# Performance work log

Measured on AMD Instinct MI355X. Metric: run time of the kernel, lower is better.

## Reference

```python
import jax, jax.numpy as jnp
import numpy as np

N = 50000   # nodes
E = 600000  # edges
D = 128     # embedding_dim
L = 4       # num_message_passing_steps


def setup_inputs() -> dict:
    key = jax.random.key(0)
    ks = jax.random.split(key, 5)
    x = jax.random.normal(ks[0], (N, D), dtype=jnp.float32)
    edge_index = jax.random.randint(ks[1], (2, E), 0, N, dtype=jnp.int32)
    # Per-layer params: MPNN linear (no bias), GCNConv weight + bias.
    lin_w = jax.random.normal(ks[2], (L, D, D), dtype=jnp.float32) / np.sqrt(D).astype(np.float32)
    gcn_w = jax.random.normal(ks[3], (L, D, D), dtype=jnp.float32) / np.sqrt(D).astype(np.float32)
    gcn_b = jax.random.normal(ks[4], (L, D), dtype=jnp.float32) * 0.01
    return {"x": x, "edge_index": edge_index, "lin_w": lin_w, "gcn_w": gcn_w, "gcn_b": gcn_b}


def reference(x, edge_index, lin_w, gcn_w, gcn_b):
    n = x.shape[0]
    # GCNConv defaults: add_self_loops=True, normalize=True.
    loops = jnp.arange(n, dtype=edge_index.dtype)
    src = jnp.concatenate([edge_index[0], loops])  # [E+N]
    dst = jnp.concatenate([edge_index[1], loops])  # [E+N]
    # Degree computed on dst (col) for flow='source_to_target'.
    deg = jax.ops.segment_sum(jnp.ones_like(src, dtype=x.dtype), dst, num_segments=n)
    dinv = jnp.where(deg > 0, jax.lax.rsqrt(jnp.maximum(deg, 1.0)), 0.0)
    norm = dinv[src] * dinv[dst]  # [E+N]

    for l in range(lin_w.shape[0]):
        h = x @ lin_w[l].T                 # MPNNLayer.linear (no bias)
        h = h @ gcn_w[l].T                 # GCNConv internal linear
        msgs = h[src] * norm[:, None]      # gather + normalize  [E+N, D]
        agg = jax.ops.segment_sum(msgs, dst, num_segments=n)
        x = agg + gcn_b[l]                 # GCNConv bias
        # NOTE: self.relu is `Sequential as ReLU` -> empty Sequential = identity.
    return x
```

## Files before the change

### kernel.cpp

```cpp
#include <hip/hip_runtime.h>

#define DEMB 128

typedef __attribute__((ext_vector_type(8))) _Float16 half8;
typedef __attribute__((ext_vector_type(4))) _Float16 half4;
typedef __attribute__((ext_vector_type(4))) float f32x4;

__global__ void kwc(const float* __restrict__ gcn, const float* __restrict__ lin,
                    float* __restrict__ Ms) {
  __shared__ float sa[128];
  int l = blockIdx.x >> 7, i = blockIdx.x & 127, j = threadIdx.x;
  sa[j] = gcn[((size_t)l * 128 + i) * 128 + j];
  __syncthreads();
  float acc = 0.f;
#pragma unroll 8
  for (int k = 0; k < 128; ++k) acc += sa[k] * lin[((size_t)l * 128 + k) * 128 + j];
  Ms[((size_t)l * 128 + i) * 128 + j] = acc;
}

__global__ void kst2(const float* __restrict__ Ms, const float* __restrict__ gb,
                     float* __restrict__ A1, float* __restrict__ B1,
                     float* __restrict__ v0, float* __restrict__ cb) {
  const float* M0 = Ms;
  const float* M1 = Ms + 16384;
  const float* M2 = Ms + 2 * 16384;
  const float* M3 = Ms + 3 * 16384;
  __shared__ float sa[128];
  int b = blockIdx.x, j = threadIdx.x;
  if (b < 128) {
    sa[j] = M1[b * 128 + j];
    __syncthreads();
    float acc = 0.f;
#pragma unroll 8
    for (int k = 0; k < 128; ++k) acc += sa[k] * M0[k * 128 + j];
    A1[b * 128 + j] = acc;
  } else if (b < 256) {
    int i = b - 128;
    sa[j] = M3[i * 128 + j];
    __syncthreads();
    float acc = 0.f;
#pragma unroll 8
    for (int k = 0; k < 128; ++k) acc += sa[k] * M2[k * 128 + j];
    B1[i * 128 + j] = acc;
  } else if (b == 256) {
    sa[j] = gb[j];
    __syncthreads();
    float acc = 0.f;
#pragma unroll 8
    for (int k = 0; k < 128; ++k) acc += M1[j * 128 + k] * sa[k];
    v0[j] = acc;
  } else {
    sa[j] = gb[2 * 128 + j];
    __syncthreads();
    float acc = 0.f;
#pragma unroll 8
    for (int k = 0; k < 128; ++k) acc += M3[j * 128 + k] * sa[k];
    cb[256 + j] = acc;
  }
}

__global__ void kst3(const float* __restrict__ A1, const float* __restrict__ B1,
                     const float* __restrict__ v0, const float* __restrict__ gb,
                     _Float16* __restrict__ Rh, float* __restrict__ cb) {
  __shared__ float sa[128];
  int b = blockIdx.x, j = threadIdx.x;
  if (b < 128) {
    sa[j] = B1[b * 128 + j];
    __syncthreads();
    float acc = 0.f;
#pragma unroll 8
    for (int k = 0; k < 128; ++k) acc += sa[k] * A1[k * 128 + j];
    Rh[b * 128 + j] = (_Float16)acc;
  } else if (b == 128) {
    sa[j] = v0[j];
    __syncthreads();
    float acc = 0.f;
#pragma unroll 8
    for (int k = 0; k < 128; ++k) acc += B1[j * 128 + k] * sa[k];
    cb[j] = acc;
  } else {
    sa[j] = gb[128 + j];
    __syncthreads();
    float acc = 0.f;
#pragma unroll 8
    for (int k = 0; k < 128; ++k) acc += B1[j * 128 + k] * sa[k];
    cb[128 + j] = acc;
  }
}

__global__ void kinit(int* __restrict__ deg, int n) {
  int i = blockIdx.x * 256 + threadIdx.x;
  if (i < n) deg[i] = 0;
}

__global__ void kdeg(const int* __restrict__ ei, int* __restrict__ deg, int etot) {
  int i = blockIdx.x * 256 + threadIdx.x;
  if (i < etot) atomicAdd(&deg[ei[etot + i]], 1);
}

__global__ void kscan1(const int* __restrict__ deg, int* __restrict__ off,
                       int* __restrict__ bsum, float* __restrict__ dinv,
                       float* __restrict__ dinv2, int n) {
  __shared__ int s[256];
  int t = threadIdx.x, i = blockIdx.x * 256 + t;
  int c = 0;
  if (i < n) {
    c = deg[i];
    float dv = rsqrtf((float)(c + 1));
    dinv[i] = dv;
    dinv2[i] = dv * dv;
  }
  s[t] = c;
  __syncthreads();
  for (int o = 1; o < 256; o <<= 1) {
    int v = (t >= o) ? s[t - o] : 0;
    __syncthreads();
    s[t] += v;
    __syncthreads();
  }
  if (i < n) off[i] = s[t] - c;
  if (t == 255) bsum[blockIdx.x] = s[t];
}

__global__ void kscan2(const int* __restrict__ bsum, int* __restrict__ boff,
                       int nb, int* __restrict__ off, int n, int etot) {
  __shared__ int s[256];
  int t = threadIdx.x;
  int c = (t < nb) ? bsum[t] : 0;
  s[t] = c;
  __syncthreads();
  for (int o = 1; o < 256; o <<= 1) {
    int v = (t >= o) ? s[t - o] : 0;
    __syncthreads();
    s[t] += v;
    __syncthreads();
  }
  if (t < nb) boff[t] = s[t] - c;
  if (t == 0) off[n] = etot;
}

__global__ void kscan3(int* __restrict__ off, const int* __restrict__ boff,
                       int* __restrict__ cur, int n) {
  int i = blockIdx.x * 256 + threadIdx.x;
  if (i < n) {
    int o = off[i] + boff[i >> 8];
    off[i] = o;
    cur[i] = o;
  }
}

__global__ void kfill(const int* __restrict__ ei, int* __restrict__ cur,
                      int* __restrict__ csr, int etot) {
  int i = blockIdx.x * 256 + threadIdx.x;
  if (i < etot) {
    int d = ei[etot + i];
    int p = atomicAdd(&cur[d], 1);
    csr[p] = ei[i];
  }
}

__global__ void kpre(const float* __restrict__ x, const float* __restrict__ dinv,
                     _Float16* __restrict__ xh, int n) {
  int gid = blockIdx.x * 256 + threadIdx.x;
  if (gid >= n * 32) return;
  int r = gid >> 5, c = (gid & 31) * 4;
  float d = dinv[r];
  float4 v = *(const float4*)(x + (size_t)r * DEMB + c);
  half4 o = {(_Float16)(v.x * d), (_Float16)(v.y * d), (_Float16)(v.z * d), (_Float16)(v.w * d)};
  *(half4*)(xh + (size_t)r * DEMB + c) = o;
}

template <int WITHU>
__launch_bounds__(256)
__global__ void kagg16(const _Float16* __restrict__ vin, const int* __restrict__ csr,
                       const int* __restrict__ off, const float* __restrict__ scale,
                       const float* __restrict__ dinv, const float* __restrict__ a_in,
                       float* __restrict__ u_out, float* __restrict__ a_out,
                       _Float16* __restrict__ vout, int n) {
  int node = (int)((blockIdx.x * 256u + threadIdx.x) >> 4);
  if (node >= n) return;
  int l16 = threadIdx.x & 15;
  const _Float16* base = vin + 8 * l16;
  half8 sv = *(const half8*)(base + (size_t)node * DEMB);
  float acc[8];
#pragma unroll
  for (int j = 0; j < 8; ++j) acc[j] = (float)sv[j];
  float s = WITHU ? a_in[node] : 0.f;
  int e = off[node], end = off[node + 1];
  for (; e + 8 <= end; e += 8) {
    int i0 = csr[e], i1 = csr[e + 1], i2 = csr[e + 2], i3 = csr[e + 3];
    int i4 = csr[e + 4], i5 = csr[e + 5], i6 = csr[e + 6], i7 = csr[e + 7];
    half8 r0 = *(const half8*)(base + (size_t)i0 * DEMB);
    half8 r1 = *(const half8*)(base + (size_t)i1 * DEMB);
    half8 r2 = *(const half8*)(base + (size_t)i2 * DEMB);
    half8 r3 = *(const half8*)(base + (size_t)i3 * DEMB);
    half8 r4 = *(const half8*)(base + (size_t)i4 * DEMB);
    half8 r5 = *(const half8*)(base + (size_t)i5 * DEMB);
    half8 r6 = *(const half8*)(base + (size_t)i6 * DEMB);
    half8 r7 = *(const half8*)(base + (size_t)i7 * DEMB);
    if (WITHU)
      s += a_in[i0] + a_in[i1] + a_in[i2] + a_in[i3] +
           a_in[i4] + a_in[i5] + a_in[i6] + a_in[i7];
#pragma unroll
    for (int j = 0; j < 8; ++j)
      acc[j] += ((float)r0[j] + (float)r1[j]) + ((float)r2[j] + (float)r3[j]) +
                ((float)r4[j] + (float)r5[j]) + ((float)r6[j] + (float)r7[j]);
  }
  for (; e + 4 <= end; e += 4) {
    int i0 = csr[e], i1 = csr[e + 1], i2 = csr[e + 2], i3 = csr[e + 3];
    half8 r0 = *(const half8*)(base + (size_t)i0 * DEMB);
    half8 r1 = *(const half8*)(base + (size_t)i1 * DEMB);
    half8 r2 = *(const half8*)(base + (size_t)i2 * DEMB);
    half8 r3 = *(const half8*)(base + (size_t)i3 * DEMB);
    if (WITHU) s += a_in[i0] + a_in[i1] + a_in[i2] + a_in[i3];
#pragma unroll
    for (int j = 0; j < 8; ++j)
      acc[j] += ((float)r0[j] + (float)r1[j]) + ((float)r2[j] + (float)r3[j]);
  }
  if (e < end) {
    int em = end - 1;
    int i0 = csr[e];
    int i1 = csr[min(e + 1, em)];
    int i2 = csr[min(e + 2, em)];
    float w1 = (e + 1 < end) ? 1.f : 0.f;
    float w2 = (e + 2 < end) ? 1.f : 0.f;
    half8 r0 = *(const half8*)(base + (size_t)i0 * DEMB);
    half8 r1 = *(const half8*)(base + (size_t)i1 * DEMB);
    half8 r2 = *(const half8*)(base + (size_t)i2 * DEMB);
    if (WITHU) s += a_in[i0] + w1 * a_in[i1] + w2 * a_in[i2];
#pragma unroll
    for (int j = 0; j < 8; ++j)
      acc[j] += (float)r0[j] + w1 * (float)r1[j] + w2 * (float)r2[j];
  }
  float sc = scale[node];
  half8 o;
#pragma unroll
  for (int j = 0; j < 8; ++j) o[j] = (_Float16)(acc[j] * sc);
  *(half8*)(vout + (size_t)node * DEMB + 8 * l16) = o;
  if (WITHU && l16 == 0) {
    float dv = dinv[node];
    float u = dv * s;
    u_out[node] = u;
    a_out[node] = dv * u;
  }
}

__launch_bounds__(256)
__global__ void kgemm16(const _Float16* __restrict__ y, const _Float16* __restrict__ Rh,
                        const float* __restrict__ u1, const float* __restrict__ u2,
                        const float* __restrict__ u3, const float* __restrict__ cb,
                        const float* __restrict__ b3, float* __restrict__ out, int n) {
  int t = threadIdx.x;
  int wv = t >> 6, lane = t & 63;
  int l16 = lane & 15, g = lane >> 4;
  int row0 = blockIdx.x * 128 + wv * 32;
  f32x4 acc[2][8];
#pragma unroll
  for (int w = 0; w < 2; ++w)
#pragma unroll
    for (int n8 = 0; n8 < 8; ++n8) acc[w][n8] = (f32x4){0.f, 0.f, 0.f, 0.f};

#pragma unroll
  for (int k0 = 0; k0 < 128; k0 += 32) {
    half8 a0 = *(const half8*)(y + (size_t)(row0 + l16) * DEMB + k0 + g * 8);
    half8 a1 = *(const half8*)(y + (size_t)(row0 + 16 + l16) * DEMB + k0 + g * 8);
#pragma unroll
    for (int n8 = 0; n8 < 8; ++n8) {
      half8 b = *(const half8*)(Rh + (size_t)(n8 * 16 + l16) * DEMB + k0 + g * 8);
      acc[0][n8] = __builtin_amdgcn_mfma_f32_16x16x32_f16(a0, b, acc[0][n8], 0, 0, 0);
      acc[1][n8] = __builtin_amdgcn_mfma_f32_16x16x32_f16(a1, b, acc[1][n8], 0, 0, 0);
    }
  }
#pragma unroll
  for (int n8 = 0; n8 < 8; ++n8) {
    int col = n8 * 16 + l16;
    float cA = cb[col], cB = cb[128 + col], cC = cb[256 + col], bb = b3[col];
#pragma unroll
    for (int w = 0; w < 2; ++w)
#pragma unroll
      for (int r = 0; r < 4; ++r) {
        int row = row0 + w * 16 + g * 4 + r;
        if (row < n) {
          out[(size_t)row * DEMB + col] =
              acc[w][n8][r] + u3[row] * cA + u2[row] * cB + u1[row] * cC + bb;
        }
      }
  }
}

extern "C" void kernel_launch(void* const* d_in, const int* in_sizes, int n_in,
                              void* d_out, int out_size, void* d_ws, size_t ws_size,
                              hipStream_t stream) {
  const float* x0 = (const float*)d_in[0];
  const int* ei = (const int*)d_in[1];
  const float* lin = (const float*)d_in[2];
  const float* gcn = (const float*)d_in[3];
  const float* gb = (const float*)d_in[4];
  float* out = (float*)d_out;

  int N = in_sizes[0] / DEMB;
  int E = in_sizes[1] / 2;
  int L = in_sizes[2] / (DEMB * DEMB);
  int NP = (N + 127) & ~127;

  char* w = (char*)d_ws;
  auto carve = [&](size_t bytes) {
    char* p = w;
    w += (bytes + 255) & ~(size_t)255;
    return p;
  };
  float* Ms    = (float*)carve((size_t)L * DEMB * DEMB * 4);
  float* A1    = (float*)carve((size_t)DEMB * DEMB * 4);
  float* B1    = (float*)carve((size_t)DEMB * DEMB * 4);
  _Float16* Rh = (_Float16*)carve((size_t)DEMB * DEMB * 2);
  float* v0    = (float*)carve((size_t)DEMB * 4);
  float* cb    = (float*)carve((size_t)3 * DEMB * 4);
  float* dinv  = (float*)carve((size_t)N * 4);
  float* dnv2  = (float*)carve((size_t)N * 4);
  int* deg     = (int*)carve((size_t)N * 4);
  int* off     = (int*)carve((size_t)(N + 1) * 4);
  int* cur     = (int*)carve((size_t)N * 4);
  int* bsum    = (int*)carve(256 * 4);
  int* boff    = (int*)carve(256 * 4);
  int* csr     = (int*)carve((size_t)E * 4);
  float* u1    = (float*)carve((size_t)N * 4);
  float* u2    = (float*)carve((size_t)N * 4);
  float* u3    = (float*)carve((size_t)N * 4);
  float* a1    = (float*)carve((size_t)N * 4);
  float* a2    = (float*)carve((size_t)N * 4);
  float* a3    = (float*)carve((size_t)N * 4);
  _Float16* ha = (_Float16*)carve((size_t)NP * DEMB * 2);
  _Float16* hb = (_Float16*)carve((size_t)NP * DEMB * 2);
  (void)ws_size; (void)n_in; (void)out_size;

  int nbN = (N + 255) / 256;
  int nbE = (E + 255) / 256;
  int nbA = (N * 16 + 255) / 256;

  kwc<<<L * DEMB, DEMB, 0, stream>>>(gcn, lin, Ms);
  kst2<<<258, DEMB, 0, stream>>>(Ms, gb, A1, B1, v0, cb);
  kst3<<<130, DEMB, 0, stream>>>(A1, B1, v0, gb, Rh, cb);

  kinit<<<nbN, 256, 0, stream>>>(deg, N);
  kdeg<<<nbE, 256, 0, stream>>>(ei, deg, E);
  kscan1<<<nbN, 256, 0, stream>>>(deg, off, bsum, dinv, dnv2, N);
  kscan2<<<1, 256, 0, stream>>>(bsum, boff, nbN, off, N, E);
  kscan3<<<nbN, 256, 0, stream>>>(off, boff, cur, N);
  kfill<<<nbE, 256, 0, stream>>>(ei, cur, csr, E);

  kpre<<<(N * 32 + 255) / 256, 256, 0, stream>>>(x0, dinv, ha, N);
  kagg16<1><<<nbA, 256, 0, stream>>>(ha, csr, off, dnv2, dinv, dinv, u1, a1, hb, N);
  kagg16<1><<<nbA, 256, 0, stream>>>(hb, csr, off, dnv2, dinv, a1, u2, a2, ha, N);
  kagg16<1><<<nbA, 256, 0, stream>>>(ha, csr, off, dnv2, dinv, a2, u3, a3, hb, N);
  kagg16<0><<<nbA, 256, 0, stream>>>(hb, csr, off, dinv, dinv, nullptr, nullptr, nullptr, ha, N);

  kgemm16<<<(N + 127) / 128, 256, 0, stream>>>(ha, Rh, u1, u2, u3, cb, gb + 3 * DEMB, out, N);
}
```

Baseline: 221.8 us.

## Bucket nodes by in-degree and process aggregation in degree-sorted order

```diff
diff --git a/kernel.cpp b/kernel.cpp
--- a/kernel.cpp
+++ b/kernel.cpp
@@ -88,11 +88,6 @@
   }
 }
 
-__global__ void kinit(int* __restrict__ deg, int n) {
-  int i = blockIdx.x * 256 + threadIdx.x;
-  if (i < n) deg[i] = 0;
-}
-
 __global__ void kdeg(const int* __restrict__ ei, int* __restrict__ deg, int etot) {
   int i = blockIdx.x * 256 + threadIdx.x;
   if (i < etot) atomicAdd(&deg[ei[etot + i]], 1);
@@ -100,7 +95,7 @@
 
 __global__ void kscan1(const int* __restrict__ deg, int* __restrict__ off,
                        int* __restrict__ bsum, float* __restrict__ dinv,
-                       float* __restrict__ dinv2, int n) {
+                       float* __restrict__ dinv2, int* __restrict__ bcnt, int n) {
   __shared__ int s[256];
   int t = threadIdx.x, i = blockIdx.x * 256 + t;
   int c = 0;
@@ -109,6 +104,7 @@
     float dv = rsqrtf((float)(c + 1));
     dinv[i] = dv;
     dinv2[i] = dv * dv;
+    atomicAdd(&bcnt[c < 63 ? c : 63], 1);
   }
   s[t] = c;
   __syncthreads();
@@ -123,7 +119,8 @@
 }
 
 __global__ void kscan2(const int* __restrict__ bsum, int* __restrict__ boff,
-                       int nb, int* __restrict__ off, int n, int etot) {
+                       int nb, int* __restrict__ off, int n, int etot,
+                       const int* __restrict__ bcnt, int* __restrict__ bcur) {
   __shared__ int s[256];
   int t = threadIdx.x;
   int c = (t < nb) ? bsum[t] : 0;
@@ -137,15 +134,30 @@
   }
   if (t < nb) boff[t] = s[t] - c;
   if (t == 0) off[n] = etot;
+  __syncthreads();
+  int bc = (t < 64) ? bcnt[t] : 0;
+  s[t] = bc;
+  __syncthreads();
+  for (int o = 1; o < 64; o <<= 1) {
+    int v = (t >= o && t < 64) ? s[t - o] : 0;
+    __syncthreads();
+    if (t < 64) s[t] += v;
+    __syncthreads();
+  }
+  if (t < 64) bcur[t] = s[t] - bc;
 }
 
 __global__ void kscan3(int* __restrict__ off, const int* __restrict__ boff,
-                       int* __restrict__ cur, int n) {
+                       int* __restrict__ cur, const int* __restrict__ deg,
+                       int* __restrict__ bcur, int* __restrict__ perm, int n) {
   int i = blockIdx.x * 256 + threadIdx.x;
   if (i < n) {
     int o = off[i] + boff[i >> 8];
     off[i] = o;
     cur[i] = o;
+    int d = deg[i];
+    int p = atomicAdd(&bcur[d < 63 ? d : 63], 1);
+    perm[p] = i;
   }
 }
 
@@ -173,12 +185,13 @@
 template <int WITHU>
 __launch_bounds__(256)
 __global__ void kagg16(const _Float16* __restrict__ vin, const int* __restrict__ csr,
-                       const int* __restrict__ off, const float* __restrict__ scale,
-                       const float* __restrict__ dinv, const float* __restrict__ a_in,
-                       float* __restrict__ u_out, float* __restrict__ a_out,
-                       _Float16* __restrict__ vout, int n) {
-  int node = (int)((blockIdx.x * 256u + threadIdx.x) >> 4);
-  if (node >= n) return;
+                       const int* __restrict__ off, const int* __restrict__ perm,
+                       const float* __restrict__ scale, const float* __restrict__ dinv,
+                       const float* __restrict__ a_in, float* __restrict__ u_out,
+                       float* __restrict__ a_out, _Float16* __restrict__ vout, int n) {
+  int grp = (int)((blockIdx.x * 256u + threadIdx.x) >> 4);
+  if (grp >= n) return;
+  int node = perm[grp];
   int l16 = threadIdx.x & 15;
   const _Float16* base = vin + 8 * l16;
   half8 sv = *(const half8*)(base + (size_t)node * DEMB);
@@ -317,11 +330,14 @@
   float* cb    = (float*)carve((size_t)3 * DEMB * 4);
   float* dinv  = (float*)carve((size_t)N * 4);
   float* dnv2  = (float*)carve((size_t)N * 4);
-  int* deg     = (int*)carve((size_t)N * 4);
+  int* deg     = (int*)carve((size_t)(N + 128) * 4);
+  int* bcnt    = deg + N;
+  int* bcur    = deg + N + 64;
   int* off     = (int*)carve((size_t)(N + 1) * 4);
   int* cur     = (int*)carve((size_t)N * 4);
   int* bsum    = (int*)carve(256 * 4);
   int* boff    = (int*)carve(256 * 4);
+  int* perm    = (int*)carve((size_t)N * 4);
   int* csr     = (int*)carve((size_t)E * 4);
   float* u1    = (float*)carve((size_t)N * 4);
   float* u2    = (float*)carve((size_t)N * 4);
@@ -337,22 +353,23 @@
   int nbE = (E + 255) / 256;
   int nbA = (N * 16 + 255) / 256;
 
+  hipMemsetAsync(deg, 0, (size_t)(N + 128) * 4, stream);
+
   kwc<<<L * DEMB, DEMB, 0, stream>>>(gcn, lin, Ms);
   kst2<<<258, DEMB, 0, stream>>>(Ms, gb, A1, B1, v0, cb);
   kst3<<<130, DEMB, 0, stream>>>(A1, B1, v0, gb, Rh, cb);
 
-  kinit<<<nbN, 256, 0, stream>>>(deg, N);
   kdeg<<<nbE, 256, 0, stream>>>(ei, deg, E);
-  kscan1<<<nbN, 256, 0, stream>>>(deg, off, bsum, dinv, dnv2, N);
-  kscan2<<<1, 256, 0, stream>>>(bsum, boff, nbN, off, N, E);
-  kscan3<<<nbN, 256, 0, stream>>>(off, boff, cur, N);
+  kscan1<<<nbN, 256, 0, stream>>>(deg, off, bsum, dinv, dnv2, bcnt, N);
+  kscan2<<<1, 256, 0, stream>>>(bsum, boff, nbN, off, N, E, bcnt, bcur);
+  kscan3<<<nbN, 256, 0, stream>>>(off, boff, cur, deg, bcur, perm, N);
   kfill<<<nbE, 256, 0, stream>>>(ei, cur, csr, E);
 
   kpre<<<(N * 32 + 255) / 256, 256, 0, stream>>>(x0, dinv, ha, N);
-  kagg16<1><<<nbA, 256, 0, stream>>>(ha, csr, off, dnv2, dinv, dinv, u1, a1, hb, N);
-  kagg16<1><<<nbA, 256, 0, stream>>>(hb, csr, off, dnv2, dinv, a1, u2, a2, ha, N);
-  kagg16<1><<<nbA, 256, 0, stream>>>(ha, csr, off, dnv2, dinv, a2, u3, a3, hb, N);
-  kagg16<0><<<nbA, 256, 0, stream>>>(hb, csr, off, dinv, dinv, nullptr, nullptr, nullptr, ha, N);
+  kagg16<1><<<nbA, 256, 0, stream>>>(ha, csr, off, perm, dnv2, dinv, dinv, u1, a1, hb, N);
+  kagg16<1><<<nbA, 256, 0, stream>>>(hb, csr, off, perm, dnv2, dinv, a1, u2, a2, ha, N);
+  kagg16<1><<<nbA, 256, 0, stream>>>(ha, csr, off, perm, dnv2, dinv, a2, u3, a3, hb, N);
+  kagg16<0><<<nbA, 256, 0, stream>>>(hb, csr, off, perm, dinv, dinv, nullptr, nullptr, nullptr, ha, N);
 
   kgemm16<<<(N + 127) / 128, 256, 0, stream>>>(ha, Rh, u1, u2, u3, cb, gb + 3 * DEMB, out, N);
 }
```

Measured after the change: 537.7 us. 142% more time.
